# Kernel tuning notes

Measured on AMD Instinct MI355X. Metric: run time of the kernel, lower is better.

## Reference

```python
import jax, jax.numpy as jnp
import numpy as np

B, H, P, K, E, BN = 8, 256, 1024, 32, 4, 64


def setup_inputs() -> dict:
    key = jax.random.key(0)
    ks = jax.random.split(key, 8)
    current = jax.random.normal(ks[0], (B, H, P), dtype=jnp.float32)
    neighbor_features = jax.random.normal(ks[1], (B, H, P, K), dtype=jnp.float32)
    # binary {0,1} validity mask, stored as float like the torch module expects
    neighbor_validity = jax.random.randint(ks[2], (B, 1, P, K), 0, 2).astype(jnp.float32)
    edge_features = jax.random.normal(ks[3], (B, E, P, K), dtype=jnp.float32)
    # 1x1 Conv2d weights flattened to matrices: (out_ch, in_ch)
    w1 = jax.random.normal(ks[4], (BN, 2 * H + E), dtype=jnp.float32) * 0.05
    b1 = jnp.zeros((BN,), dtype=jnp.float32)
    w2 = jax.random.normal(ks[5], (BN,), dtype=jnp.float32) * 0.05  # second conv: out_ch=1
    b2 = jnp.zeros((), dtype=jnp.float32)
    return {
        "current": current,
        "neighbor_features": neighbor_features,
        "neighbor_validity": neighbor_validity,
        "edge_features": edge_features,
        "w1": w1,
        "b1": b1,
        "w2": w2,
        "b2": b2,
    }


def reference(current, neighbor_features, neighbor_validity, edge_features, w1, b1, w2, b2):
    h_dim = current.shape[1]
    # Split the 1x1-conv weight along the concat axis so we never materialize
    # the [B, 2H+E, P, K] concatenated tensor (same math as cat + conv1x1).
    w1c = w1[:, :h_dim]            # acts on broadcast center features
    w1n = w1[:, h_dim:2 * h_dim]   # acts on neighbor features
    w1e = w1[:, 2 * h_dim:]        # acts on edge features

    hid = (
        jnp.einsum("bcp,oc->bop", current, w1c)[:, :, :, None]
        + jnp.einsum("bcpk,oc->bopk", neighbor_features, w1n)
        + jnp.einsum("bcpk,oc->bopk", edge_features, w1e)
        + b1[None, :, None, None]
    )
    hid = jax.nn.relu(hid)                                  # (B, BN, P, K)
    logits = jnp.einsum("bopk,o->bpk", hid, w2) + b2        # (B, P, K)

    valid = neighbor_validity[:, 0] > 0.5                   # (B, P, K) bool
    logits = jnp.where(valid, logits, -jnp.inf)
    has_any = jnp.any(valid, axis=-1, keepdims=True)        # (B, P, 1)
    logits_safe = jnp.where(has_any, logits, 0.0)           # all-masked rows -> 0 logits
    weights = jax.nn.softmax(logits_safe, axis=-1)
    weights = jnp.where(has_any & valid, weights, 0.0)      # zero weight on pads / empty rows

    pooled = jnp.einsum("bcpk,bpk->bcp", neighbor_features, weights)
    return pooled
```

## Files before the change

### kernel.cpp

```cpp
#include <hip/hip_runtime.h>
#include <math.h>


#define B_ 8
#define H_ 256
#define P_ 1024
#define K_ 32
#define E_ 4
#define BN_ 64

typedef __attribute__((ext_vector_type(8))) short short8;
typedef __attribute__((ext_vector_type(4))) float floatx4;

__device__ __forceinline__ unsigned short bf16_rne(float f) {
  unsigned u = __float_as_uint(f);
  u += 0x7fffu + ((u >> 16) & 1u);
  return (unsigned short)(u >> 16);
}
__device__ __forceinline__ unsigned pack_bf16(float lo, float hi) {
  unsigned r;
  asm("v_cvt_pk_bf16_f32 %0, %1, %2" : "=v"(r) : "v"(lo), "v"(hi));
  return r;
}

__device__ __forceinline__ unsigned* tile_ptr(unsigned* tile, int n, int cp) {
  return tile + n * 128 + ((((cp >> 2) ^ (n & 7)) << 2) | (cp & 3));
}

__global__ __launch_bounds__(256) void prep_kernel(
    const float* __restrict__ w1, unsigned short* __restrict__ w1m) {
  int i = blockIdx.x * 256 + threadIdx.x;
  if (i >= 4 * 17 * 64 * 8) return;
  int j = i & 7, lane = (i >> 3) & 63;
  int kt = i >> 9;
  int mt = kt / 17, ki = kt % 17;
  int o = mt * 16 + (lane & 15);
  int c = ki * 32 + (lane >> 4) * 8 + j;
  float v = (c < 516) ? w1[o * 516 + c] : 0.f;
  w1m[i] = bf16_rne(v);
}

__global__ __launch_bounds__(256, 2) void soft_attn_agg_kernel(
    const float* __restrict__ cur,
    const float* __restrict__ nf,
    const float* __restrict__ nv,
    const float* __restrict__ ef,
    const unsigned short* __restrict__ w1m,
    const float* __restrict__ b1,
    const float* __restrict__ w2,
    float* __restrict__ out) {
  __shared__ unsigned s_tile[128 * 128];
  __shared__ unsigned short s_curb[4][264];
  __shared__ unsigned s_edge[4][32][2];
  __shared__ float s_b1v[BN_];
  __shared__ float s_w2v[BN_];
  __shared__ float s_lg[128];
  __shared__ float s_wt[128];

  const int t = threadIdx.x;
  const unsigned bid = blockIdx.x;
  const unsigned xcd = bid & 7u, sx = bid >> 3;
  const int b = (int)(sx >> 5);
  const int pg = (int)(xcd * 32u + (sx & 31u));
  const int p0 = pg * 4;

  const int w = t >> 6;
  const int lane = t & 63;
  const int q = lane >> 4;
  const int ln15 = lane & 15;

  const int PKr = P_ * K_;
  const float* nf_b = nf + ((size_t)b * H_ * P_ + p0) * K_;

  float4 ca = *(const float4*)(cur + ((size_t)b * H_ + t) * P_ + p0);
  float sv = 0.f, e0 = 0.f, e1 = 0.f, e2 = 0.f, e3 = 0.f, bw = 0.f;
  if (t < 128) {
    sv = nv[((size_t)b * P_ + p0) * K_ + t];
    const int pl = t >> 5, k = t & 31;
    const float* ep = ef + ((size_t)b * E_ * P_ + p0 + pl) * K_ + k;
    e0 = ep[0];
    e1 = ep[(size_t)PKr];
    e2 = ep[(size_t)(2 * PKr)];
    e3 = ep[(size_t)(3 * PKr)];
  } else if (t < 192) {
    bw = b1[t - 128];
  } else {
    bw = w2[t - 192];
  }

  float ve0[32], ve1[32], vo0[32], vo1[32];
#define ISSUE_CH(ch)                                       \
  {                                                        \
    const float* re = nf_b + (size_t)(8 * (ch) + 2 * w) * PKr; \
    const float* ro = re + PKr;                            \
    ve0[ch] = re[lane];                                    \
    ve1[ch] = re[lane + 64];                               \
    vo0[ch] = ro[lane];                                    \
    vo1[ch] = ro[lane + 64];                               \
  }
#define CONSUME_CH(ch)                                     \
  {                                                        \
    unsigned pk0 = pack_bf16(ve0[ch], vo0[ch]);            \
    unsigned pk1 = pack_bf16(ve1[ch], vo1[ch]);            \
    const int cpv = 4 * (ch) + w;                          \
    *tile_ptr(s_tile, lane, cpv) = pk0;                    \
    *tile_ptr(s_tile, lane + 64, cpv) = pk1;               \
  }

#pragma unroll
  for (int ch = 0; ch < 8; ++ch) ISSUE_CH(ch);
  __builtin_amdgcn_sched_barrier(0);

  s_curb[0][t] = bf16_rne(ca.x);
  s_curb[1][t] = bf16_rne(ca.y);
  s_curb[2][t] = bf16_rne(ca.z);
  s_curb[3][t] = bf16_rne(ca.w);
  float my_valid = sv;
  if (t < 128) {
    const int pl = t >> 5, k = t & 31;
    s_edge[pl][k][0] = pack_bf16(e0, e1);
    s_edge[pl][k][1] = pack_bf16(e2, e3);
  } else if (t < 192) {
    s_b1v[t - 128] = bw;
  } else {
    s_w2v[t - 192] = bw;
  }
  __builtin_amdgcn_sched_barrier(0);

#pragma unroll
  for (int ch = 0; ch < 32; ++ch) {
    if (ch < 24) ISSUE_CH(ch + 8);
    CONSUME_CH(ch);
    __builtin_amdgcn_sched_barrier(0);
  }
  __syncthreads();

  floatx4 acc[4][2];
#pragma unroll
  for (int mt = 0; mt < 4; ++mt) {
    floatx4 binit = *(const floatx4*)&s_b1v[mt * 16 + q * 4];
    acc[mt][0] = binit;
    acc[mt][1] = binit;
  }
  const unsigned short* w1m_l = w1m + (size_t)lane * 8;

#pragma unroll
  for (int ki = 0; ki < 8; ++ki) {
    short8 bc = *(const short8*)&s_curb[w][ki * 32 + q * 8];
#pragma unroll
    for (int mt = 0; mt < 4; ++mt) {
      short8 a = *(const short8*)(w1m_l + (size_t)(mt * 17 + ki) * 512);
      acc[mt][0] = __builtin_amdgcn_mfma_f32_16x16x32_bf16(a, bc, acc[mt][0], 0, 0, 0);
      acc[mt][1] = __builtin_amdgcn_mfma_f32_16x16x32_bf16(a, bc, acc[mt][1], 0, 0, 0);
    }
  }
#pragma unroll
  for (int ck = 0; ck < 8; ++ck) {
    short8 bn0 = *(const short8*)tile_ptr(s_tile, 32 * w + ln15, (4 * ck + q) << 2);
    short8 bn1 = *(const short8*)tile_ptr(s_tile, 32 * w + 16 + ln15, (4 * ck + q) << 2);
#pragma unroll
    for (int mt = 0; mt < 4; ++mt) {
      short8 a = *(const short8*)(w1m_l + (size_t)(mt * 17 + 8 + ck) * 512);
      acc[mt][0] = __builtin_amdgcn_mfma_f32_16x16x32_bf16(a, bn0, acc[mt][0], 0, 0, 0);
      acc[mt][1] = __builtin_amdgcn_mfma_f32_16x16x32_bf16(a, bn1, acc[mt][1], 0, 0, 0);
    }
  }
  {
    union { unsigned u[4]; short8 s; } ub0, ub1;
    *(uint2*)&ub0.u[0] = *(const uint2*)&s_edge[w][ln15][0];
    ub0.u[2] = 0u; ub0.u[3] = 0u;
    *(uint2*)&ub1.u[0] = *(const uint2*)&s_edge[w][16 + ln15][0];
    ub1.u[2] = 0u; ub1.u[3] = 0u;
#pragma unroll
    for (int mt = 0; mt < 4; ++mt) {
      short8 a = *(const short8*)(w1m_l + (size_t)(mt * 17 + 16) * 512);
      acc[mt][0] = __builtin_amdgcn_mfma_f32_16x16x32_bf16(a, ub0.s, acc[mt][0], 0, 0, 0);
      acc[mt][1] = __builtin_amdgcn_mfma_f32_16x16x32_bf16(a, ub1.s, acc[mt][1], 0, 0, 0);
    }
  }

#pragma unroll
  for (int nti = 0; nti < 2; ++nti) {
    float lp = 0.f;
#pragma unroll
    for (int mt = 0; mt < 4; ++mt) {
      const floatx4 w2v = *(const floatx4*)&s_w2v[mt * 16 + q * 4];
#pragma unroll
      for (int r = 0; r < 4; ++r)
        lp = fmaf(fmaxf(acc[mt][nti][r], 0.f), w2v[r], lp);
    }
    lp += __shfl_xor(lp, 16);
    lp += __shfl_xor(lp, 32);
    if (lane < 16) s_lg[(2 * w + nti) * 16 + ln15] = lp;
  }
  __syncthreads();

  if (t < 128) {
    float lg = s_lg[t];
    bool v = my_valid > 0.5f;
    float ml = v ? lg : -INFINITY;
#pragma unroll
    for (int m = 1; m < 32; m <<= 1) ml = fmaxf(ml, __shfl_xor(ml, m));
    float e = v ? __expf(lg - ml) : 0.f;
    float ssum = e;
#pragma unroll
    for (int m = 1; m < 32; m <<= 1) ssum += __shfl_xor(ssum, m);
    s_wt[t] = (ml > -INFINITY) ? (e / ssum) : 0.f;
  }
  __syncthreads();

  {
    const int cpr = t & 127, ph = t >> 7;
    const int nb = ph * 64;
    float a0e = 0.f, a0o = 0.f, a1e = 0.f, a1o = 0.f;
#pragma unroll
    for (int k = 0; k < K_; ++k) {
      const unsigned u0 = *tile_ptr(s_tile, nb + k, cpr);
      const unsigned u1 = *tile_ptr(s_tile, nb + 32 + k, cpr);
      const float wt0 = s_wt[nb + k];
      const float wt1 = s_wt[nb + 32 + k];
      a0e = fmaf(__uint_as_float(u0 << 16), wt0, a0e);
      a0o = fmaf(__uint_as_float(u0 & 0xffff0000u), wt0, a0o);
      a1e = fmaf(__uint_as_float(u1 << 16), wt1, a1e);
      a1o = fmaf(__uint_as_float(u1 & 0xffff0000u), wt1, a1o);
    }
    float* op = out + ((size_t)b * H_ + 2 * cpr) * P_ + p0 + 2 * ph;
    float2 ve; ve.x = a0e; ve.y = a1e;
    float2 vo; vo.x = a0o; vo.y = a1o;
    *(float2*)op = ve;
    *(float2*)(op + P_) = vo;
  }
}

extern "C" void kernel_launch(void* const* d_in, const int* in_sizes, int n_in,
                              void* d_out, int out_size, void* d_ws,
                              size_t ws_size, hipStream_t stream) {
  const float* cur = (const float*)d_in[0];
  const float* nf  = (const float*)d_in[1];
  const float* nv  = (const float*)d_in[2];
  const float* ef  = (const float*)d_in[3];
  const float* w1  = (const float*)d_in[4];
  const float* b1  = (const float*)d_in[5];
  const float* w2  = (const float*)d_in[6];

  unsigned short* w1m = (unsigned short*)d_ws;
  prep_kernel<<<(4 * 17 * 64 * 8 + 255) / 256, 256, 0, stream>>>(w1, w1m);
  soft_attn_agg_kernel<<<B_ * P_ / 4, 256, 0, stream>>>(
      cur, nf, nv, ef, w1m, b1, w2, (float*)d_out);
}
```

Before: 397.0 us.

## Halve points per block and split hidden channels across waves for occupancy

Each block now handles 2 points instead of 4, which halves the LDS tile and the register prefetch arrays so four blocks can fit per CU instead of two. The MFMA work is re-split so each wave owns one 16-row slice of the hidden dimension over all 64 neighbor columns, rather than all 64 hidden rows over 32 columns. Per-wave partial logits are then summed through shared memory. The aim is more latency hiding for the streaming neighbor-feature loads. The cost is twice as many blocks, with the weight and current-feature setup repeated per block, and narrower output stores.

After: 396.0 us. No clear change (-0.2%).

```diff
diff --git a/kernel.cpp b/kernel.cpp
--- a/kernel.cpp
+++ b/kernel.cpp
@@ -40,7 +40,7 @@
   w1m[i] = bf16_rne(v);
 }
 
-__global__ __launch_bounds__(256, 2) void soft_attn_agg_kernel(
+__global__ __launch_bounds__(256, 4) void soft_attn_agg_kernel(
     const float* __restrict__ cur,
     const float* __restrict__ nf,
     const float* __restrict__ nv,
@@ -49,20 +49,20 @@
     const float* __restrict__ b1,
     const float* __restrict__ w2,
     float* __restrict__ out) {
-  __shared__ unsigned s_tile[128 * 128];
-  __shared__ unsigned short s_curb[4][264];
-  __shared__ unsigned s_edge[4][32][2];
+  __shared__ unsigned s_tile[64 * 128];
+  __shared__ unsigned short s_curb[2][264];
+  __shared__ unsigned s_edge[2][32][2];
   __shared__ float s_b1v[BN_];
   __shared__ float s_w2v[BN_];
-  __shared__ float s_lg[128];
-  __shared__ float s_wt[128];
+  __shared__ float s_lgp[4][64];
+  __shared__ float s_wt[64];
 
   const int t = threadIdx.x;
   const unsigned bid = blockIdx.x;
   const unsigned xcd = bid & 7u, sx = bid >> 3;
-  const int b = (int)(sx >> 5);
-  const int pg = (int)(xcd * 32u + (sx & 31u));
-  const int p0 = pg * 4;
+  const int b = (int)(sx >> 6);
+  const int pg = (int)(xcd * 64u + (sx & 63u));
+  const int p0 = pg * 2;
 
   const int w = t >> 6;
   const int lane = t & 63;
@@ -72,9 +72,9 @@
   const int PKr = P_ * K_;
   const float* nf_b = nf + ((size_t)b * H_ * P_ + p0) * K_;
 
-  float4 ca = *(const float4*)(cur + ((size_t)b * H_ + t) * P_ + p0);
+  float2 ca = *(const float2*)(cur + ((size_t)b * H_ + t) * P_ + p0);
   float sv = 0.f, e0 = 0.f, e1 = 0.f, e2 = 0.f, e3 = 0.f, bw = 0.f;
-  if (t < 128) {
+  if (t < 64) {
     sv = nv[((size_t)b * P_ + p0) * K_ + t];
     const int pl = t >> 5, k = t & 31;
     const float* ep = ef + ((size_t)b * E_ * P_ + p0 + pl) * K_ + k;
@@ -82,29 +82,23 @@
     e1 = ep[(size_t)PKr];
     e2 = ep[(size_t)(2 * PKr)];
     e3 = ep[(size_t)(3 * PKr)];
+  } else if (t < 128) {
+    bw = b1[t - 64];
   } else if (t < 192) {
-    bw = b1[t - 128];
-  } else {
-    bw = w2[t - 192];
-  }
-
-  float ve0[32], ve1[32], vo0[32], vo1[32];
-#define ISSUE_CH(ch)                                       \
-  {                                                        \
+    bw = w2[t - 128];
+  }
+
+  float ve[32], vo[32];
+#define ISSUE_CH(ch)                                           \
+  {                                                            \
     const float* re = nf_b + (size_t)(8 * (ch) + 2 * w) * PKr; \
-    const float* ro = re + PKr;                            \
-    ve0[ch] = re[lane];                                    \
-    ve1[ch] = re[lane + 64];                               \
-    vo0[ch] = ro[lane];                                    \
-    vo1[ch] = ro[lane + 64];                               \
-  }
-#define CONSUME_CH(ch)                                     \
-  {                                                        \
-    unsigned pk0 = pack_bf16(ve0[ch], vo0[ch]);            \
-    unsigned pk1 = pack_bf16(ve1[ch], vo1[ch]);            \
-    const int cpv = 4 * (ch) + w;                          \
-    *tile_ptr(s_tile, lane, cpv) = pk0;                    \
-    *tile_ptr(s_tile, lane + 64, cpv) = pk1;               \
+    ve[ch] = re[lane];                                         \
+    vo[ch] = re[PKr + lane];                                   \
+  }
+#define CONSUME_CH(ch)                                         \
+  {                                                            \
+    unsigned pk = pack_bf16(ve[ch], vo[ch]);                   \
+    *tile_ptr(s_tile, lane, 4 * (ch) + w) = pk;                \
   }
 
 #pragma unroll
@@ -113,17 +107,14 @@
 
   s_curb[0][t] = bf16_rne(ca.x);
   s_curb[1][t] = bf16_rne(ca.y);
-  s_curb[2][t] = bf16_rne(ca.z);
-  s_curb[3][t] = bf16_rne(ca.w);
   float my_valid = sv;
-  if (t < 128) {
-    const int pl = t >> 5, k = t & 31;
-    s_edge[pl][k][0] = pack_bf16(e0, e1);
-    s_edge[pl][k][1] = pack_bf16(e2, e3);
+  if (t < 64) {
+    s_edge[t >> 5][t & 31][0] = pack_bf16(e0, e1);
+    s_edge[t >> 5][t & 31][1] = pack_bf16(e2, e3);
+  } else if (t < 128) {
+    s_b1v[t - 64] = bw;
   } else if (t < 192) {
-    s_b1v[t - 128] = bw;
-  } else {
-    s_w2v[t - 192] = bw;
+    s_w2v[t - 128] = bw;
   }
   __builtin_amdgcn_sched_barrier(0);
 
@@ -135,68 +126,60 @@
   }
   __syncthreads();
 
-  floatx4 acc[4][2];
-#pragma unroll
-  for (int mt = 0; mt < 4; ++mt) {
-    floatx4 binit = *(const floatx4*)&s_b1v[mt * 16 + q * 4];
-    acc[mt][0] = binit;
-    acc[mt][1] = binit;
-  }
-  const unsigned short* w1m_l = w1m + (size_t)lane * 8;
+  floatx4 acc[4];
+  {
+    const floatx4 binit = *(const floatx4*)&s_b1v[16 * w + 4 * q];
+    acc[0] = binit; acc[1] = binit; acc[2] = binit; acc[3] = binit;
+  }
+  const unsigned short* w1m_w = w1m + (size_t)(w * 17) * 512 + (size_t)lane * 8;
 
 #pragma unroll
   for (int ki = 0; ki < 8; ++ki) {
-    short8 bc = *(const short8*)&s_curb[w][ki * 32 + q * 8];
-#pragma unroll
-    for (int mt = 0; mt < 4; ++mt) {
-      short8 a = *(const short8*)(w1m_l + (size_t)(mt * 17 + ki) * 512);
-      acc[mt][0] = __builtin_amdgcn_mfma_f32_16x16x32_bf16(a, bc, acc[mt][0], 0, 0, 0);
-      acc[mt][1] = __builtin_amdgcn_mfma_f32_16x16x32_bf16(a, bc, acc[mt][1], 0, 0, 0);
-    }
+    short8 a = *(const short8*)(w1m_w + (size_t)ki * 512);
+    short8 bc0 = *(const short8*)&s_curb[0][ki * 32 + q * 8];
+    short8 bc1 = *(const short8*)&s_curb[1][ki * 32 + q * 8];
+    acc[0] = __builtin_amdgcn_mfma_f32_16x16x32_bf16(a, bc0, acc[0], 0, 0, 0);
+    acc[1] = __builtin_amdgcn_mfma_f32_16x16x32_bf16(a, bc0, acc[1], 0, 0, 0);
+    acc[2] = __builtin_amdgcn_mfma_f32_16x16x32_bf16(a, bc1, acc[2], 0, 0, 0);
+    acc[3] = __builtin_amdgcn_mfma_f32_16x16x32_bf16(a, bc1, acc[3], 0, 0, 0);
   }
 #pragma unroll
   for (int ck = 0; ck < 8; ++ck) {
-    short8 bn0 = *(const short8*)tile_ptr(s_tile, 32 * w + ln15, (4 * ck + q) << 2);
-    short8 bn1 = *(const short8*)tile_ptr(s_tile, 32 * w + 16 + ln15, (4 * ck + q) << 2);
-#pragma unroll
-    for (int mt = 0; mt < 4; ++mt) {
-      short8 a = *(const short8*)(w1m_l + (size_t)(mt * 17 + 8 + ck) * 512);
-      acc[mt][0] = __builtin_amdgcn_mfma_f32_16x16x32_bf16(a, bn0, acc[mt][0], 0, 0, 0);
-      acc[mt][1] = __builtin_amdgcn_mfma_f32_16x16x32_bf16(a, bn1, acc[mt][1], 0, 0, 0);
-    }
-  }
-  {
-    union { unsigned u[4]; short8 s; } ub0, ub1;
-    *(uint2*)&ub0.u[0] = *(const uint2*)&s_edge[w][ln15][0];
-    ub0.u[2] = 0u; ub0.u[3] = 0u;
-    *(uint2*)&ub1.u[0] = *(const uint2*)&s_edge[w][16 + ln15][0];
-    ub1.u[2] = 0u; ub1.u[3] = 0u;
-#pragma unroll
-    for (int mt = 0; mt < 4; ++mt) {
-      short8 a = *(const short8*)(w1m_l + (size_t)(mt * 17 + 16) * 512);
-      acc[mt][0] = __builtin_amdgcn_mfma_f32_16x16x32_bf16(a, ub0.s, acc[mt][0], 0, 0, 0);
-      acc[mt][1] = __builtin_amdgcn_mfma_f32_16x16x32_bf16(a, ub1.s, acc[mt][1], 0, 0, 0);
-    }
-  }
-
-#pragma unroll
-  for (int nti = 0; nti < 2; ++nti) {
-    float lp = 0.f;
-#pragma unroll
-    for (int mt = 0; mt < 4; ++mt) {
-      const floatx4 w2v = *(const floatx4*)&s_w2v[mt * 16 + q * 4];
+    short8 a = *(const short8*)(w1m_w + (size_t)(8 + ck) * 512);
+#pragma unroll
+    for (int nt = 0; nt < 4; ++nt) {
+      short8 bn = *(const short8*)tile_ptr(s_tile, 16 * nt + ln15, (4 * ck + q) << 2);
+      acc[nt] = __builtin_amdgcn_mfma_f32_16x16x32_bf16(a, bn, acc[nt], 0, 0, 0);
+    }
+  }
+  {
+    short8 ae = *(const short8*)(w1m_w + (size_t)16 * 512);
+#pragma unroll
+    for (int nt = 0; nt < 4; ++nt) {
+      union { unsigned u[4]; short8 s; } ub;
+      *(uint2*)&ub.u[0] = *(const uint2*)&s_edge[nt >> 1][(nt & 1) * 16 + ln15][0];
+      ub.u[2] = 0u; ub.u[3] = 0u;
+      acc[nt] = __builtin_amdgcn_mfma_f32_16x16x32_bf16(ae, ub.s, acc[nt], 0, 0, 0);
+    }
+  }
+
+  {
+    const floatx4 w2v = *(const floatx4*)&s_w2v[16 * w + 4 * q];
+#pragma unroll
+    for (int nt = 0; nt < 4; ++nt) {
+      float lp = 0.f;
 #pragma unroll
       for (int r = 0; r < 4; ++r)
-        lp = fmaf(fmaxf(acc[mt][nti][r], 0.f), w2v[r], lp);
-    }
-    lp += __shfl_xor(lp, 16);
-    lp += __shfl_xor(lp, 32);
-    if (lane < 16) s_lg[(2 * w + nti) * 16 + ln15] = lp;
+        lp = fmaf(fmaxf(acc[nt][r], 0.f), w2v[r], lp);
+      lp += __shfl_xor(lp, 16);
+      lp += __shfl_xor(lp, 32);
+      if (lane < 16) s_lgp[w][16 * nt + ln15] = lp;
+    }
   }
   __syncthreads();
 
-  if (t < 128) {
-    float lg = s_lg[t];
+  if (t < 64) {
+    float lg = s_lgp[0][t] + s_lgp[1][t] + s_lgp[2][t] + s_lgp[3][t];
     bool v = my_valid > 0.5f;
     float ml = v ? lg : -INFINITY;
 #pragma unroll
@@ -211,24 +194,18 @@
 
   {
     const int cpr = t & 127, ph = t >> 7;
-    const int nb = ph * 64;
-    float a0e = 0.f, a0o = 0.f, a1e = 0.f, a1o = 0.f;
+    const int nb = 32 * ph;
+    float a_e = 0.f, a_o = 0.f;
 #pragma unroll
     for (int k = 0; k < K_; ++k) {
-      const unsigned u0 = *tile_ptr(s_tile, nb + k, cpr);
-      const unsigned u1 = *tile_ptr(s_tile, nb + 32 + k, cpr);
-      const float wt0 = s_wt[nb + k];
-      const float wt1 = s_wt[nb + 32 + k];
-      a0e = fmaf(__uint_as_float(u0 << 16), wt0, a0e);
-      a0o = fmaf(__uint_as_float(u0 & 0xffff0000u), wt0, a0o);
-      a1e = fmaf(__uint_as_float(u1 << 16), wt1, a1e);
-      a1o = fmaf(__uint_as_float(u1 & 0xffff0000u), wt1, a1o);
-    }
-    float* op = out + ((size_t)b * H_ + 2 * cpr) * P_ + p0 + 2 * ph;
-    float2 ve; ve.x = a0e; ve.y = a1e;
-    float2 vo; vo.x = a0o; vo.y = a1o;
-    *(float2*)op = ve;
-    *(float2*)(op + P_) = vo;
+      const unsigned u = *tile_ptr(s_tile, nb + k, cpr);
+      const float wt = s_wt[nb + k];
+      a_e = fmaf(__uint_as_float(u << 16), wt, a_e);
+      a_o = fmaf(__uint_as_float(u & 0xffff0000u), wt, a_o);
+    }
+    float* op = out + ((size_t)b * H_ + 2 * cpr) * P_ + p0 + ph;
+    *op = a_e;
+    *(op + P_) = a_o;
   }
 }
 
@@ -245,6 +222,6 @@
 
   unsigned short* w1m = (unsigned short*)d_ws;
   prep_kernel<<<(4 * 17 * 64 * 8 + 255) / 256, 256, 0, stream>>>(w1, w1m);
-  soft_attn_agg_kernel<<<B_ * P_ / 4, 256, 0, stream>>>(
+  soft_attn_agg_kernel<<<B_ * P_ / 2, 256, 0, stream>>>(
       cur, nf, nv, ef, w1m, b1, w2, (float*)d_out);
 }
```
